# Optimization experiments

Measured on AMD Instinct MI355X. Metric: run time of the kernel, lower is better.

## Reference

```python
import jax, jax.numpy as jnp
import numpy as np

T, H, I, E, TOP_K = 4096, 2048, 768, 16, 2


def _pack_i2s(tern):
    # tern: int8 in {-1,0,1}, shape [..., K] with K % 4 == 0
    m = (tern + 1).astype(jnp.uint8)  # map to {0,1,2}
    m = m.reshape(*tern.shape[:-1], -1, 4)
    return (m[..., 0] | (m[..., 1] << 2) | (m[..., 2] << 4) | (m[..., 3] << 6)).astype(jnp.uint8)


def _quantize_alpha(alpha):
    # per-column alpha -> int8 with global scale (quantize_alpha_int8)
    scale = jnp.maximum(jnp.abs(alpha).max(), 1e-8) / 127.0
    q = jnp.clip(jnp.round(alpha / scale), -128, 127).astype(jnp.int8)
    return q, scale.astype(jnp.float32)


def _unpack_i2s(packed, K, alpha):
    # packed: uint8 [..., N, K//4]; alpha: [..., K] per input column
    shifts = jnp.array([0, 2, 4, 6], dtype=jnp.uint8)
    ext = (packed[..., None] >> shifts) & jnp.uint8(3)  # [..., N, K//4, 4]
    vals = ext.reshape(*packed.shape[:-1], K).astype(jnp.float32) - 1.0  # {-1,0,1}
    return vals * alpha[..., None, :]


def setup_inputs() -> dict:
    key = jax.random.key(0)
    ks = jax.random.split(key, 6)
    x = jax.random.normal(ks[0], (T, H), dtype=jnp.float32)
    router_logits = jax.random.normal(ks[1], (T, E), dtype=jnp.float32)
    tern13 = jax.random.randint(ks[2], (E, 2 * I, H), -1, 2, dtype=jnp.int8)
    tern2 = jax.random.randint(ks[3], (E, H, I), -1, 2, dtype=jnp.int8)
    a13 = jax.random.uniform(ks[4], (E, H), minval=0.01, maxval=0.05, dtype=jnp.float32)
    a2 = jax.random.uniform(ks[5], (E, I), minval=0.01, maxval=0.05, dtype=jnp.float32)
    w13_alpha_q, w13_alpha_scale = _quantize_alpha(a13)
    w2_alpha_q, w2_alpha_scale = _quantize_alpha(a2)
    return {
        "x": x,
        "router_logits": router_logits,
        "w13_packed": _pack_i2s(tern13),
        "w13_alpha_q": w13_alpha_q,
        "w13_alpha_scale": w13_alpha_scale,
        "w2_packed": _pack_i2s(tern2),
        "w2_alpha_q": w2_alpha_q,
        "w2_alpha_scale": w2_alpha_scale,
    }


def reference(x, router_logits, w13_packed, w13_alpha_q, w13_alpha_scale,
              w2_packed, w2_alpha_q, w2_alpha_scale):
    # dequant int8 alphas, then dequant 2-bit ternary weights
    a13 = w13_alpha_q.astype(jnp.float32) * w13_alpha_scale  # [E, H]
    a2 = w2_alpha_q.astype(jnp.float32) * w2_alpha_scale     # [E, I]
    w13 = _unpack_i2s(w13_packed, H, a13)  # [E, 2I, H]
    w2 = _unpack_i2s(w2_packed, I, a2)     # [E, H, I]

    # top-k routing with renormalized softmax weights
    probs = jax.nn.softmax(router_logits, axis=-1)
    topw, topi = jax.lax.top_k(probs, TOP_K)           # [T, k]
    topw = topw / topw.sum(axis=-1, keepdims=True)
    combine = jnp.sum(jax.nn.one_hot(topi, E, dtype=x.dtype) * topw[..., None], axis=1)  # [T, E]

    # grouped expert matmuls (dense dispatch over experts)
    gu = jnp.einsum('th,enh->ten', x, w13)             # [T, E, 2I]
    gate, up = jnp.split(gu, 2, axis=-1)
    act = jax.nn.silu(gate) * up                       # [T, E, I]
    down = jnp.einsum('tei,ehi->teh', act, w2)         # [T, E, H]
    return jnp.einsum('te,teh->th', combine, down)     # [T, H]
```

## Files before the change

kernel.cpp:

```cpp
#include <hip/hip_runtime.h>
#include <stdint.h>

#define T_TOK 4096
#define HDIM  2048
#define IDIM  768
#define NEXP  16
#define NPAIR (T_TOK * 2)
#define PAIR_CAP (NPAIR + 256)

typedef float f32x4 __attribute__((ext_vector_type(4)));
typedef __bf16 bf16x8 __attribute__((ext_vector_type(8)));
typedef unsigned short u16x8 __attribute__((ext_vector_type(8)));
typedef unsigned int u32;
typedef const __attribute__((address_space(1))) u32* as1_u32p;
typedef __attribute__((address_space(3))) u32* as3_u32p;

__device__ __forceinline__ unsigned short f2bf(float f) {
  u32 u = __float_as_uint(f);
  u += 0x7FFFu + ((u >> 16) & 1u);
  return (unsigned short)(u >> 16);
}

__device__ __forceinline__ unsigned short tb(int m) {
  return m == 0 ? (unsigned short)0xBF80 : (m == 2 ? (unsigned short)0x3F80 : (unsigned short)0);
}

__device__ __forceinline__ f32x4 mfma16(bf16x8 a, bf16x8 b, f32x4 c) {
  return __builtin_amdgcn_mfma_f32_16x16x32_bf16(a, b, c, 0, 0, 0);
}

__global__ __launch_bounds__(256) void route_kernel(
    const float* __restrict__ logits, int* __restrict__ counts,
    int* __restrict__ t2i, float* __restrict__ t2w) {
  const int t = blockIdx.x * 256 + threadIdx.x;
  if (t >= T_TOK) return;
  const float* l = logits + t * NEXP;
  float m0 = -1e30f, m1 = -1e30f;
  int i0 = 0, i1 = 0;
#pragma unroll
  for (int j = 0; j < NEXP; ++j) {
    const float v = l[j];
    if (v > m0) { m1 = m0; i1 = i0; m0 = v; i0 = j; }
    else if (v > m1) { m1 = v; i1 = j; }
  }
  const float w0 = 1.0f / (1.0f + expf(m1 - m0));
  t2i[t] = i0 | (i1 << 8);
  t2w[t] = w0;
  atomicAdd(&counts[i0], 1);
  atomicAdd(&counts[i1], 1);
}

__global__ void scan_kernel(const int* __restrict__ counts,
                            int* __restrict__ offs, int* __restrict__ cursor) {
  if (threadIdx.x == 0) {
    int s = 0;
    for (int e = 0; e < NEXP; ++e) { offs[e] = s; cursor[e] = s; s += counts[e]; }
    offs[NEXP] = s;
  }
}

__global__ __launch_bounds__(256) void fill_kernel(
    const int* __restrict__ t2i, const float* __restrict__ t2w,
    int* __restrict__ cursor, int* __restrict__ pair_token,
    float* __restrict__ pair_wt, int* __restrict__ pair_eid,
    int* __restrict__ t2p0, int* __restrict__ t2p1) {
  const int t = blockIdx.x * 256 + threadIdx.x;
  if (t >= T_TOK) return;
  const int ii = t2i[t];
  const float w0 = t2w[t];
  const int i0 = ii & 255, i1 = (ii >> 8) & 255;
  const int p0 = atomicAdd(&cursor[i0], 1);
  pair_token[p0] = t; pair_wt[p0] = w0; pair_eid[p0] = i0;
  const int p1 = atomicAdd(&cursor[i1], 1);
  pair_token[p1] = t; pair_wt[p1] = 1.0f - w0; pair_eid[p1] = i1;
  t2p0[t] = p0; t2p1[t] = p1;
}

__global__ __launch_bounds__(256) void repack_kernel(
    const int* __restrict__ w, u32* __restrict__ o) {
  const int j0 = (blockIdx.x * 256 + threadIdx.x) * 4;
  const int4* w4 = (const int4*)w;
  uint4 r;
#pragma unroll
  for (int k = 0; k < 4; ++k) {
    const int4 a = w4[j0 + k];
    ((u32*)&r)[k] = (u32)(a.x & 255) | ((u32)(a.y & 255) << 8) |
                    ((u32)(a.z & 255) << 16) | ((u32)(a.w & 255) << 24);
  }
  ((uint4*)o)[blockIdx.x * 256 + threadIdx.x] = r;
}

__global__ __launch_bounds__(256) void xg_kernel(
    const float* __restrict__ x, const int* __restrict__ a13q,
    const float* __restrict__ s13p, const int* __restrict__ pair_token,
    const int* __restrict__ pair_eid, unsigned short* __restrict__ xg) {
  const int p = blockIdx.x;
  const int t = pair_token[p];
  const int e = pair_eid[p];
  const float s13 = *s13p;
  const int h0 = threadIdx.x * 8;
  const float* xp = x + (size_t)t * HDIM + h0;
  const int* ap = a13q + (size_t)e * HDIM + h0;
  const float4 x0 = ((const float4*)xp)[0];
  const float4 x1 = ((const float4*)xp)[1];
  const int4 a0 = ((const int4*)ap)[0];
  const int4 a1 = ((const int4*)ap)[1];
  u16x8 q;
  q[0] = f2bf(x0.x * (float)a0.x * s13);
  q[1] = f2bf(x0.y * (float)a0.y * s13);
  q[2] = f2bf(x0.z * (float)a0.z * s13);
  q[3] = f2bf(x0.w * (float)a0.w * s13);
  q[4] = f2bf(x1.x * (float)a1.x * s13);
  q[5] = f2bf(x1.y * (float)a1.y * s13);
  q[6] = f2bf(x1.z * (float)a1.z * s13);
  q[7] = f2bf(x1.w * (float)a1.w * s13);
  *(u16x8*)(xg + (size_t)p * HDIM + h0) = q;
}

__global__ __launch_bounds__(256, 3) void gemm1_kernel(
    const u32* __restrict__ wq13, const int* __restrict__ a2q,
    const float* __restrict__ s2p, const int* __restrict__ counts,
    const int* __restrict__ offs, const unsigned short* __restrict__ xg,
    unsigned short* __restrict__ act) {
  const int nT = blockIdx.x;
  const int mT = blockIdx.y;
  const int e  = blockIdx.z;
  const int cnt = counts[e];
  if (mT * 128 >= cnt) return;
  const int base = offs[e];
  const int tid = threadIdx.x;

  __shared__ unsigned short sA[128 * 32];
  __shared__ unsigned short sB[128 * 40];
  __shared__ uint2 lut[256];

  {
    const int b = tid;
    const u32 lo = (u32)tb(b & 3) | ((u32)tb((b >> 2) & 3) << 16);
    const u32 hi = (u32)tb((b >> 4) & 3) | ((u32)tb((b >> 6) & 3) << 16);
    lut[b] = make_uint2(lo, hi);
  }
  __syncthreads();

  const int wave = tid >> 6, lane = tid & 63;
  const int quad = lane >> 4, ln = lane & 15;

  const int bn = tid >> 1, bhalf = tid & 1;
  const int grow = (bn < 64) ? (nT * 64 + bn) : (IDIM + nT * 64 + (bn - 64));
  const u32* bptr = wq13 + ((size_t)e * (2 * IDIM) + grow) * (HDIM / 16) + bhalf;
  unsigned short* sBw = sB + bn * 40 + (bhalf << 4);

  const int arow = lane >> 2;
  const int acol = (lane & 3) * 8;
  const size_t arow0 = (size_t)(base + mT * 128);

  f32x4 acc[2][8] = {};

  for (int kt = 0; kt < HDIM / 32; ++kt) {
#pragma unroll
    for (int c = 0; c < 2; ++c) {
      const unsigned short* gp =
          xg + (arow0 + c * 64 + wave * 16 + arow) * HDIM + kt * 32 + acol;
      unsigned short* lp = sA + (c * 64 + wave * 16) * 32;
      __builtin_amdgcn_global_load_lds((as1_u32p)(const void*)gp, (as3_u32p)(void*)lp, 16, 0, 0);
    }
    {
      const u32 wb = bptr[kt * 2];
      const uint2 q0 = lut[wb & 255], q1 = lut[(wb >> 8) & 255];
      const uint2 q2 = lut[(wb >> 16) & 255], q3 = lut[wb >> 24];
      *(uint2*)(sBw + 0) = q0;
      *(uint2*)(sBw + 4) = q1;
      *(uint2*)(sBw + 8) = q2;
      *(uint2*)(sBw + 12) = q3;
    }
    __syncthreads();
    bf16x8 af[2];
#pragma unroll
    for (int mi = 0; mi < 2; ++mi)
      af[mi] = *(const bf16x8*)(sA + (wave * 32 + mi * 16 + ln) * 32 + quad * 8);
#pragma unroll
    for (int ni = 0; ni < 8; ++ni) {
      const bf16x8 bf = *(const bf16x8*)(sB + (ni * 16 + ln) * 40 + quad * 8);
      acc[0][ni] = mfma16(af[0], bf, acc[0][ni]);
      acc[1][ni] = mfma16(af[1], bf, acc[1][ni]);
    }
    __syncthreads();
  }

  const float s2 = *s2p;
#pragma unroll
  for (int ni = 0; ni < 4; ++ni) {
    const int i = nT * 64 + ni * 16 + ln;
    const float a2v = (float)a2q[e * IDIM + i] * s2;
#pragma unroll
    for (int mi = 0; mi < 2; ++mi) {
      const f32x4 g = acc[mi][ni];
      const f32x4 u = acc[mi][ni + 4];
#pragma unroll
      for (int r = 0; r < 4; ++r) {
        const int m = mT * 128 + wave * 32 + mi * 16 + quad * 4 + r;
        if (m < cnt) {
          const float gv = g[r];
          const float av = gv / (1.0f + __expf(-gv)) * u[r];
          act[(size_t)(base + m) * IDIM + i] = f2bf(av * a2v);
        }
      }
    }
  }
}

template <bool ATOMIC>
__global__ __launch_bounds__(256, 3) void gemm2_kernel(
    const u32* __restrict__ wq2, const int* __restrict__ counts,
    const int* __restrict__ offs, const int* __restrict__ pair_token,
    const float* __restrict__ pair_wt, const unsigned short* __restrict__ act,
    float* __restrict__ dst) {
  const int nT = blockIdx.x;
  const int mT = blockIdx.y;
  const int e  = blockIdx.z;
  const int cnt = counts[e];
  if (mT * 128 >= cnt) return;
  const int base = offs[e];
  const int tid = threadIdx.x;

  __shared__ unsigned short sA[128 * 32];
  __shared__ unsigned short sB[128 * 40];
  __shared__ uint2 lut[256];
  __shared__ int stok[128];
  __shared__ float swt[128];

  {
    const int b = tid;
    const u32 lo = (u32)tb(b & 3) | ((u32)tb((b >> 2) & 3) << 16);
    const u32 hi = (u32)tb((b >> 4) & 3) | ((u32)tb((b >> 6) & 3) << 16);
    lut[b] = make_uint2(lo, hi);
    if (ATOMIC && tid < 128) {
      const int m = mT * 128 + tid;
      const bool v = m < cnt;
      stok[tid] = v ? pair_token[base + m] : 0;
      swt[tid]  = v ? pair_wt[base + m] : 0.0f;
    }
  }
  __syncthreads();

  const int wave = tid >> 6, lane = tid & 63;
  const int quad = lane >> 4, ln = lane & 15;

  const int bn = tid >> 1, bhalf = tid & 1;
  const u32* bptr = wq2 + ((size_t)e * HDIM + nT * 128 + bn) * (IDIM / 16) + bhalf;
  unsigned short* sBw = sB + bn * 40 + (bhalf << 4);

  const int arow = lane >> 2;
  const int acol = (lane & 3) * 8;
  const size_t arow0 = (size_t)(base + mT * 128);

  f32x4 acc[2][8] = {};

  for (int kt = 0; kt < IDIM / 32; ++kt) {
#pragma unroll
    for (int c = 0; c < 2; ++c) {
      const unsigned short* gp =
          act + (arow0 + c * 64 + wave * 16 + arow) * IDIM + kt * 32 + acol;
      unsigned short* lp = sA + (c * 64 + wave * 16) * 32;
      __builtin_amdgcn_global_load_lds((as1_u32p)(const void*)gp, (as3_u32p)(void*)lp, 16, 0, 0);
    }
    {
      const u32 wb = bptr[kt * 2];
      const uint2 q0 = lut[wb & 255], q1 = lut[(wb >> 8) & 255];
      const uint2 q2 = lut[(wb >> 16) & 255], q3 = lut[wb >> 24];
      *(uint2*)(sBw + 0) = q0;
      *(uint2*)(sBw + 4) = q1;
      *(uint2*)(sBw + 8) = q2;
      *(uint2*)(sBw + 12) = q3;
    }
    __syncthreads();
    bf16x8 af[2];
#pragma unroll
    for (int mi = 0; mi < 2; ++mi)
      af[mi] = *(const bf16x8*)(sA + (wave * 32 + mi * 16 + ln) * 32 + quad * 8);
#pragma unroll
    for (int ni = 0; ni < 8; ++ni) {
      const bf16x8 bf = *(const bf16x8*)(sB + (ni * 16 + ln) * 40 + quad * 8);
      acc[0][ni] = mfma16(af[0], bf, acc[0][ni]);
      acc[1][ni] = mfma16(af[1], bf, acc[1][ni]);
    }
    __syncthreads();
  }

#pragma unroll
  for (int mi = 0; mi < 2; ++mi) {
#pragma unroll
    for (int r = 0; r < 4; ++r) {
      const int ml = wave * 32 + mi * 16 + quad * 4 + r;
      const int m = mT * 128 + ml;
      if (m < cnt) {
        if (ATOMIC) {
          const float wgt = swt[ml];
          float* orow = dst + (size_t)stok[ml] * HDIM + nT * 128;
#pragma unroll
          for (int ni = 0; ni < 8; ++ni)
            atomicAdd(orow + ni * 16 + ln, wgt * acc[mi][ni][r]);
        } else {
          float* drow = dst + (size_t)(base + m) * HDIM + nT * 128;
#pragma unroll
          for (int ni = 0; ni < 8; ++ni)
            drow[ni * 16 + ln] = acc[mi][ni][r];
        }
      }
    }
  }
}

__global__ __launch_bounds__(256) void combine_kernel(
    const int* __restrict__ t2p0, const int* __restrict__ t2p1,
    const float* __restrict__ t2w, const float* __restrict__ down,
    float* __restrict__ out) {
  const int t = blockIdx.x;
  const float w0 = t2w[t];
  const float w1 = 1.0f - w0;
  const float* d0 = down + (size_t)t2p0[t] * HDIM;
  const float* d1 = down + (size_t)t2p1[t] * HDIM;
  float* o = out + (size_t)t * HDIM;
  const int h = threadIdx.x * 8;
  const f32x4 a0 = *(const f32x4*)(d0 + h);
  const f32x4 a1 = *(const f32x4*)(d0 + h + 4);
  const f32x4 b0 = *(const f32x4*)(d1 + h);
  const f32x4 b1 = *(const f32x4*)(d1 + h + 4);
  *(f32x4*)(o + h) = w0 * a0 + w1 * b0;
  *(f32x4*)(o + h + 4) = w0 * a1 + w1 * b1;
}

__global__ __launch_bounds__(256, 2) void gemm1_c(
    const int* __restrict__ w13p, const int* __restrict__ a2q,
    const float* __restrict__ s2p, const int* __restrict__ counts,
    const int* __restrict__ offs, const unsigned short* __restrict__ xg,
    unsigned short* __restrict__ act) {
  const int nT = blockIdx.x, mT = blockIdx.y, e = blockIdx.z;
  const int cnt = counts[e];
  if (mT * 256 >= cnt) return;
  const int base = offs[e];
  const int tid = threadIdx.x;
  __shared__ unsigned short sA[256 * 32];
  __shared__ unsigned short sB[128 * 40];
  __shared__ uint2 lut[256];
  {
    const int b = tid;
    const u32 lo = (u32)tb(b & 3) | ((u32)tb((b >> 2) & 3) << 16);
    const u32 hi = (u32)tb((b >> 4) & 3) | ((u32)tb((b >> 6) & 3) << 16);
    lut[b] = make_uint2(lo, hi);
  }
  __syncthreads();
  const int wave = tid >> 6, lane = tid & 63;
  const int quad = lane >> 4, ln = lane & 15;
  const int bn = tid >> 1, bhalf = tid & 1;
  const int grow = (bn < 64) ? (nT * 64 + bn) : (IDIM + nT * 64 + (bn - 64));
  const int* bptr = w13p + ((size_t)e * (2 * IDIM) + grow) * (HDIM / 4) + bhalf * 4;
  unsigned short* sBw = sB + bn * 40 + (bhalf << 4);
  const int arow = lane >> 2, acol = (lane & 3) * 8;
  const size_t arow0 = (size_t)(base + mT * 256);
  f32x4 acc[4][8] = {};
  for (int kt = 0; kt < HDIM / 32; ++kt) {
#pragma unroll
    for (int c = 0; c < 4; ++c) {
      const unsigned short* gp =
          xg + (arow0 + c * 64 + wave * 16 + arow) * HDIM + kt * 32 + acol;
      unsigned short* lp = sA + (c * 64 + wave * 16) * 32;
      __builtin_amdgcn_global_load_lds((as1_u32p)(const void*)gp, (as3_u32p)(void*)lp, 16, 0, 0);
    }
    {
      const int4 wv = *(const int4*)(bptr + kt * 8);
      const uint2 q0 = lut[wv.x], q1 = lut[wv.y], q2 = lut[wv.z], q3 = lut[wv.w];
      *(uint2*)(sBw + 0) = q0; *(uint2*)(sBw + 4) = q1;
      *(uint2*)(sBw + 8) = q2; *(uint2*)(sBw + 12) = q3;
    }
    __syncthreads();
    bf16x8 af[4];
#pragma unroll
    for (int mi = 0; mi < 4; ++mi)
      af[mi] = *(const bf16x8*)(sA + (wave * 64 + mi * 16 + ln) * 32 + quad * 8);
#pragma unroll
    for (int ni = 0; ni < 8; ++ni) {
      const bf16x8 bf = *(const bf16x8*)(sB + (ni * 16 + ln) * 40 + quad * 8);
#pragma unroll
      for (int mi = 0; mi < 4; ++mi) acc[mi][ni] = mfma16(af[mi], bf, acc[mi][ni]);
    }
    __syncthreads();
  }
  const float s2 = *s2p;
#pragma unroll
  for (int ni = 0; ni < 4; ++ni) {
    const int i = nT * 64 + ni * 16 + ln;
    const float a2v = (float)a2q[e * IDIM + i] * s2;
#pragma unroll
    for (int mi = 0; mi < 4; ++mi) {
      const f32x4 g = acc[mi][ni];
      const f32x4 u = acc[mi][ni + 4];
#pragma unroll
      for (int r = 0; r < 4; ++r) {
        const int m = mT * 256 + wave * 64 + mi * 16 + quad * 4 + r;
        if (m < cnt) {
          const float gv = g[r];
          const float av = gv / (1.0f + __expf(-gv)) * u[r];
          act[(size_t)(base + m) * IDIM + i] = f2bf(av * a2v);
        }
      }
    }
  }
}

__global__ __launch_bounds__(256, 2) void gemm2_c(
    const int* __restrict__ w2p, const int* __restrict__ counts,
    const int* __restrict__ offs, const int* __restrict__ pair_token,
    const float* __restrict__ pair_wt, const unsigned short* __restrict__ act,
    float* __restrict__ out) {
  const int nT = blockIdx.x, mT = blockIdx.y, e = blockIdx.z;
  const int cnt = counts[e];
  if (mT * 256 >= cnt) return;
  const int base = offs[e];
  const int tid = threadIdx.x;
  __shared__ unsigned short sA[256 * 32];
  __shared__ unsigned short sB[128 * 40];
  __shared__ uint2 lut[256];
  __shared__ int stok[256];
  __shared__ float swt[256];
  {
    const int b = tid;
    const u32 lo = (u32)tb(b & 3) | ((u32)tb((b >> 2) & 3) << 16);
    const u32 hi = (u32)tb((b >> 4) & 3) | ((u32)tb((b >> 6) & 3) << 16);
    lut[b] = make_uint2(lo, hi);
    const int m = mT * 256 + tid;
    const bool v = m < cnt;
    stok[tid] = v ? pair_token[base + m] : 0;
    swt[tid]  = v ? pair_wt[base + m] : 0.0f;
  }
  __syncthreads();
  const int wave = tid >> 6, lane = tid & 63;
  const int quad = lane >> 4, ln = lane & 15;
  const int bn = tid >> 1, bhalf = tid & 1;
  const int* bptr = w2p + ((size_t)e * HDIM + nT * 128 + bn) * (IDIM / 4) + bhalf * 4;
  unsigned short* sBw = sB + bn * 40 + (bhalf << 4);
  const int arow = lane >> 2, acol = (lane & 3) * 8;
  const size_t arow0 = (size_t)(base + mT * 256);
  f32x4 acc[4][8] = {};
  for (int kt = 0; kt < IDIM / 32; ++kt) {
#pragma unroll
    for (int c = 0; c < 4; ++c) {
      const unsigned short* gp =
          act + (arow0 + c * 64 + wave * 16 + arow) * IDIM + kt * 32 + acol;
      unsigned short* lp = sA + (c * 64 + wave * 16) * 32;
      __builtin_amdgcn_global_load_lds((as1_u32p)(const void*)gp, (as3_u32p)(void*)lp, 16, 0, 0);
    }
    {
      const int4 wv = *(const int4*)(bptr + kt * 8);
      const uint2 q0 = lut[wv.x], q1 = lut[wv.y], q2 = lut[wv.z], q3 = lut[wv.w];
      *(uint2*)(sBw + 0) = q0; *(uint2*)(sBw + 4) = q1;
      *(uint2*)(sBw + 8) = q2; *(uint2*)(sBw + 12) = q3;
    }
    __syncthreads();
    bf16x8 af[4];
#pragma unroll
    for (int mi = 0; mi < 4; ++mi)
      af[mi] = *(const bf16x8*)(sA + (wave * 64 + mi * 16 + ln) * 32 + quad * 8);
#pragma unroll
    for (int ni = 0; ni < 8; ++ni) {
      const bf16x8 bf = *(const bf16x8*)(sB + (ni * 16 + ln) * 40 + quad * 8);
#pragma unroll
      for (int mi = 0; mi < 4; ++mi) acc[mi][ni] = mfma16(af[mi], bf, acc[mi][ni]);
    }
    __syncthreads();
  }
#pragma unroll
  for (int mi = 0; mi < 4; ++mi) {
#pragma unroll
    for (int r = 0; r < 4; ++r) {
      const int ml = wave * 64 + mi * 16 + quad * 4 + r;
      const int m = mT * 256 + ml;
      if (m < cnt) {
        const float wgt = swt[ml];
        float* orow = out + (size_t)stok[ml] * HDIM + nT * 128;
#pragma unroll
        for (int ni = 0; ni < 8; ++ni)
          atomicAdd(orow + ni * 16 + ln, wgt * acc[mi][ni][r]);
      }
    }
  }
}

extern "C" void kernel_launch(void* const* d_in, const int* in_sizes, int n_in,
                              void* d_out, int out_size, void* d_ws, size_t ws_size,
                              hipStream_t stream) {
  const float* x      = (const float*)d_in[0];
  const float* logits = (const float*)d_in[1];
  const int*   w13p   = (const int*)d_in[2];
  const int*   a13q   = (const int*)d_in[3];
  const float* s13    = (const float*)d_in[4];
  const int*   w2p    = (const int*)d_in[5];
  const int*   a2q    = (const int*)d_in[6];
  const float* s2     = (const float*)d_in[7];
  float* out = (float*)d_out;

  char* ws = (char*)d_ws;
  int*   counts     = (int*)(ws + 0);
  int*   cursor     = (int*)(ws + 64);
  int*   offs       = (int*)(ws + 128);
  int*   t2i        = (int*)(ws + 256);
  float* t2w        = (float*)(ws + 256 + 4 * T_TOK);
  int*   t2p0       = (int*)(ws + 256 + 8 * T_TOK);
  int*   t2p1       = (int*)(ws + 256 + 12 * T_TOK);
  int*   pair_token = (int*)(ws + 256 + 16 * T_TOK);
  float* pair_wt    = (float*)(ws + 256 + 16 * T_TOK + 4 * PAIR_CAP);
  int*   pair_eid   = (int*)(ws + 256 + 16 * T_TOK + 8 * PAIR_CAP);
  const size_t hdr_end = ((size_t)(256 + 16 * T_TOK + 12 * PAIR_CAP) + 255) & ~(size_t)255;

  const size_t n32_13 = (size_t)NEXP * 2 * IDIM * (HDIM / 16);
  const size_t n32_2  = (size_t)NEXP * HDIM * (IDIM / 16);
  const size_t rp13_b = n32_13 * 4, rp2_b = n32_2 * 4;
  const size_t xg_b   = (size_t)PAIR_CAP * HDIM * 2;
  const size_t act_b  = (size_t)PAIR_CAP * IDIM * 2;
  const size_t down_b = (size_t)PAIR_CAP * HDIM * 4;

  const size_t need_A = hdr_end + rp13_b + rp2_b + xg_b + act_b + down_b;
  const size_t need_B = hdr_end + rp13_b + rp2_b + xg_b + act_b;

  hipMemsetAsync(counts, 0, 256, stream);
  route_kernel<<<T_TOK / 256, 256, 0, stream>>>(logits, counts, t2i, t2w);
  scan_kernel<<<1, 64, 0, stream>>>(counts, offs, cursor);
  fill_kernel<<<T_TOK / 256, 256, 0, stream>>>(t2i, t2w, cursor, pair_token, pair_wt,
                                               pair_eid, t2p0, t2p1);

  if (ws_size >= need_B) {
    u32* rp13 = (u32*)(ws + hdr_end);
    u32* rp2  = (u32*)(ws + hdr_end + rp13_b);
    unsigned short* xg  = (unsigned short*)(ws + hdr_end + rp13_b + rp2_b);
    unsigned short* act = (unsigned short*)(ws + hdr_end + rp13_b + rp2_b + xg_b);
    repack_kernel<<<(int)(n32_13 / 1024), 256, 0, stream>>>(w13p, rp13);
    repack_kernel<<<(int)(n32_2 / 1024), 256, 0, stream>>>(w2p, rp2);
    xg_kernel<<<NPAIR, 256, 0, stream>>>(x, a13q, s13, pair_token, pair_eid, xg);
    gemm1_kernel<<<dim3(12, 32, 16), 256, 0, stream>>>(rp13, a2q, s2, counts, offs, xg, act);
    if (ws_size >= need_A) {
      float* down = (float*)(ws + need_B);
      gemm2_kernel<false><<<dim3(16, 32, 16), 256, 0, stream>>>(
          rp2, counts, offs, pair_token, pair_wt, act, down);
      combine_kernel<<<T_TOK, 256, 0, stream>>>(t2p0, t2p1, t2w, down, out);
    } else {
      hipMemsetAsync(out, 0, (size_t)out_size * sizeof(float), stream);
      gemm2_kernel<true><<<dim3(16, 32, 16), 256, 0, stream>>>(
          rp2, counts, offs, pair_token, pair_wt, act, out);
    }
  } else {
    unsigned short* xg  = (unsigned short*)(ws + hdr_end);
    unsigned short* act = (unsigned short*)(ws + hdr_end + xg_b);
    hipMemsetAsync(out, 0, (size_t)out_size * sizeof(float), stream);
    xg_kernel<<<NPAIR, 256, 0, stream>>>(x, a13q, s13, pair_token, pair_eid, xg);
    gemm1_c<<<dim3(12, 16, 16), 256, 0, stream>>>(w13p, a2q, s2, counts, offs, xg, act);
    gemm2_c<<<dim3(16, 16, 16), 256, 0, stream>>>(w2p, counts, offs, pair_token,
                                                  pair_wt, act, out);
  }
}
```

Baseline: 390.6 us.

## Use 2x2 wave tiling, XCD-aware block order, bf16 down buffer, fold routing weight

The GEMM kernels now split the 128x128 tile across waves in a 2x2 grid, so each wave does 4x4 MFMAs per k-step instead of 2x8 with more A/B fragment reuse. Blocks are launched on a flat grid remapped so tiles of the same expert spread across XCDs. Weight words are loaded as uint4 every other k-step, and the LDS B row stride changes from 40 to 36. The routing weight moves into gemm1's activation epilogue, and the down buffer is stored as bf16 so combine becomes a plain add. The fallback path without repacking is removed. Storing down in bf16 adds a rounding step, and occupancy hints rise from 3 to 4 blocks.

```diff
diff --git a/kernel.cpp b/kernel.cpp
--- a/kernel.cpp
+++ b/kernel.cpp
@@ -117,21 +117,23 @@
   *(u16x8*)(xg + (size_t)p * HDIM + h0) = q;
 }
 
-__global__ __launch_bounds__(256, 3) void gemm1_kernel(
+__global__ __launch_bounds__(256, 4) void gemm1_kernel(
     const u32* __restrict__ wq13, const int* __restrict__ a2q,
     const float* __restrict__ s2p, const int* __restrict__ counts,
-    const int* __restrict__ offs, const unsigned short* __restrict__ xg,
-    unsigned short* __restrict__ act) {
-  const int nT = blockIdx.x;
-  const int mT = blockIdx.y;
-  const int e  = blockIdx.z;
+    const int* __restrict__ offs, const float* __restrict__ pair_wt,
+    const unsigned short* __restrict__ xg, unsigned short* __restrict__ act) {
+  const int id = blockIdx.x;
+  const int xcd = id & 7, sblk = id >> 3;
+  const int nT = sblk % 12;
+  const int gg = (sblk / 12) * 8 + xcd;
+  const int e = gg & 15, mT = gg >> 4;
   const int cnt = counts[e];
   if (mT * 128 >= cnt) return;
   const int base = offs[e];
   const int tid = threadIdx.x;
 
   __shared__ unsigned short sA[128 * 32];
-  __shared__ unsigned short sB[128 * 40];
+  __shared__ unsigned short sB[128 * 36 + 8];
   __shared__ uint2 lut[256];
 
   {
@@ -143,29 +145,32 @@
   __syncthreads();
 
   const int wave = tid >> 6, lane = tid & 63;
+  const int wm = wave >> 1, wn = wave & 1;
   const int quad = lane >> 4, ln = lane & 15;
 
   const int bn = tid >> 1, bhalf = tid & 1;
   const int grow = (bn < 64) ? (nT * 64 + bn) : (IDIM + nT * 64 + (bn - 64));
-  const u32* bptr = wq13 + ((size_t)e * (2 * IDIM) + grow) * (HDIM / 16) + bhalf;
-  unsigned short* sBw = sB + bn * 40 + (bhalf << 4);
+  const u32* browp = wq13 + ((size_t)e * (2 * IDIM) + grow) * (HDIM / 16);
+  unsigned short* sBw = sB + bn * 36 + (bhalf << 4);
 
   const int arow = lane >> 2;
   const int acol = (lane & 3) * 8;
   const size_t arow0 = (size_t)(base + mT * 128);
 
-  f32x4 acc[2][8] = {};
+  f32x4 acc[4][4] = {};
+  uint4 bq;
 
   for (int kt = 0; kt < HDIM / 32; ++kt) {
+    if ((kt & 1) == 0) bq = *(const uint4*)(browp + kt * 2);
 #pragma unroll
     for (int c = 0; c < 2; ++c) {
       const unsigned short* gp =
-          xg + (arow0 + c * 64 + wave * 16 + arow) * HDIM + kt * 32 + acol;
-      unsigned short* lp = sA + (c * 64 + wave * 16) * 32;
+          xg + (arow0 + wave * 32 + c * 16 + arow) * HDIM + kt * 32 + acol;
+      unsigned short* lp = sA + (wave * 32 + c * 16) * 32;
       __builtin_amdgcn_global_load_lds((as1_u32p)(const void*)gp, (as3_u32p)(void*)lp, 16, 0, 0);
     }
     {
-      const u32 wb = bptr[kt * 2];
+      const u32 wb = (kt & 1) ? (bhalf ? bq.w : bq.z) : (bhalf ? bq.y : bq.x);
       const uint2 q0 = lut[wb & 255], q1 = lut[(wb >> 8) & 255];
       const uint2 q2 = lut[(wb >> 16) & 255], q3 = lut[wb >> 24];
       *(uint2*)(sBw + 0) = q0;
@@ -174,35 +179,39 @@
       *(uint2*)(sBw + 12) = q3;
     }
     __syncthreads();
-    bf16x8 af[2];
-#pragma unroll
-    for (int mi = 0; mi < 2; ++mi)
-      af[mi] = *(const bf16x8*)(sA + (wave * 32 + mi * 16 + ln) * 32 + quad * 8);
-#pragma unroll
-    for (int ni = 0; ni < 8; ++ni) {
-      const bf16x8 bf = *(const bf16x8*)(sB + (ni * 16 + ln) * 40 + quad * 8);
-      acc[0][ni] = mfma16(af[0], bf, acc[0][ni]);
-      acc[1][ni] = mfma16(af[1], bf, acc[1][ni]);
-    }
+    bf16x8 af[4], bf[4];
+#pragma unroll
+    for (int mi = 0; mi < 4; ++mi)
+      af[mi] = *(const bf16x8*)(sA + (wm * 64 + mi * 16 + ln) * 32 + quad * 8);
+#pragma unroll
+    for (int ni = 0; ni < 4; ++ni) {
+      const int brow = (ni < 2) ? (wn * 32 + ni * 16) : (64 + wn * 32 + (ni - 2) * 16);
+      bf[ni] = *(const bf16x8*)(sB + (brow + ln) * 36 + quad * 8);
+    }
+#pragma unroll
+    for (int ni = 0; ni < 4; ++ni)
+#pragma unroll
+      for (int mi = 0; mi < 4; ++mi) acc[mi][ni] = mfma16(af[mi], bf[ni], acc[mi][ni]);
     __syncthreads();
   }
 
   const float s2 = *s2p;
 #pragma unroll
-  for (int ni = 0; ni < 4; ++ni) {
-    const int i = nT * 64 + ni * 16 + ln;
+  for (int gi = 0; gi < 2; ++gi) {
+    const int i = nT * 64 + wn * 32 + gi * 16 + ln;
     const float a2v = (float)a2q[e * IDIM + i] * s2;
 #pragma unroll
-    for (int mi = 0; mi < 2; ++mi) {
-      const f32x4 g = acc[mi][ni];
-      const f32x4 u = acc[mi][ni + 4];
+    for (int mi = 0; mi < 4; ++mi) {
+      const f32x4 g = acc[mi][gi];
+      const f32x4 u = acc[mi][gi + 2];
 #pragma unroll
       for (int r = 0; r < 4; ++r) {
-        const int m = mT * 128 + wave * 32 + mi * 16 + quad * 4 + r;
+        const int m = mT * 128 + wm * 64 + mi * 16 + quad * 4 + r;
         if (m < cnt) {
+          const float wt = pair_wt[base + m];
           const float gv = g[r];
-          const float av = gv / (1.0f + __expf(-gv)) * u[r];
-          act[(size_t)(base + m) * IDIM + i] = f2bf(av * a2v);
+          const float av = gv / (1.0f + __expf(-gv)) * u[r] * a2v * wt;
+          act[(size_t)(base + m) * IDIM + i] = f2bf(av);
         }
       }
     }
@@ -210,24 +219,25 @@
 }
 
 template <bool ATOMIC>
-__global__ __launch_bounds__(256, 3) void gemm2_kernel(
+__global__ __launch_bounds__(256, 4) void gemm2_kernel(
     const u32* __restrict__ wq2, const int* __restrict__ counts,
     const int* __restrict__ offs, const int* __restrict__ pair_token,
-    const float* __restrict__ pair_wt, const unsigned short* __restrict__ act,
-    float* __restrict__ dst) {
-  const int nT = blockIdx.x;
-  const int mT = blockIdx.y;
-  const int e  = blockIdx.z;
+    const unsigned short* __restrict__ act, float* __restrict__ outp,
+    unsigned short* __restrict__ down) {
+  const int id = blockIdx.x;
+  const int xcd = id & 7, sblk = id >> 3;
+  const int nT = sblk & 15;
+  const int gg = (sblk >> 4) * 8 + xcd;
+  const int e = gg & 15, mT = gg >> 4;
   const int cnt = counts[e];
   if (mT * 128 >= cnt) return;
   const int base = offs[e];
   const int tid = threadIdx.x;
 
   __shared__ unsigned short sA[128 * 32];
-  __shared__ unsigned short sB[128 * 40];
+  __shared__ unsigned short sB[128 * 36 + 8];
   __shared__ uint2 lut[256];
   __shared__ int stok[128];
-  __shared__ float swt[128];
 
   {
     const int b = tid;
@@ -236,36 +246,37 @@
     lut[b] = make_uint2(lo, hi);
     if (ATOMIC && tid < 128) {
       const int m = mT * 128 + tid;
-      const bool v = m < cnt;
-      stok[tid] = v ? pair_token[base + m] : 0;
-      swt[tid]  = v ? pair_wt[base + m] : 0.0f;
+      stok[tid] = (m < cnt) ? pair_token[base + m] : 0;
     }
   }
   __syncthreads();
 
   const int wave = tid >> 6, lane = tid & 63;
+  const int wm = wave >> 1, wn = wave & 1;
   const int quad = lane >> 4, ln = lane & 15;
 
   const int bn = tid >> 1, bhalf = tid & 1;
-  const u32* bptr = wq2 + ((size_t)e * HDIM + nT * 128 + bn) * (IDIM / 16) + bhalf;
-  unsigned short* sBw = sB + bn * 40 + (bhalf << 4);
+  const u32* browp = wq2 + ((size_t)e * HDIM + nT * 128 + bn) * (IDIM / 16);
+  unsigned short* sBw = sB + bn * 36 + (bhalf << 4);
 
   const int arow = lane >> 2;
   const int acol = (lane & 3) * 8;
   const size_t arow0 = (size_t)(base + mT * 128);
 
-  f32x4 acc[2][8] = {};
+  f32x4 acc[4][4] = {};
+  uint4 bq;
 
   for (int kt = 0; kt < IDIM / 32; ++kt) {
+    if ((kt & 1) == 0) bq = *(const uint4*)(browp + kt * 2);
 #pragma unroll
     for (int c = 0; c < 2; ++c) {
       const unsigned short* gp =
-          act + (arow0 + c * 64 + wave * 16 + arow) * IDIM + kt * 32 + acol;
-      unsigned short* lp = sA + (c * 64 + wave * 16) * 32;
+          act + (arow0 + wave * 32 + c * 16 + arow) * IDIM + kt * 32 + acol;
+      unsigned short* lp = sA + (wave * 32 + c * 16) * 32;
       __builtin_amdgcn_global_load_lds((as1_u32p)(const void*)gp, (as3_u32p)(void*)lp, 16, 0, 0);
     }
     {
-      const u32 wb = bptr[kt * 2];
+      const u32 wb = (kt & 1) ? (bhalf ? bq.w : bq.z) : (bhalf ? bq.y : bq.x);
       const uint2 q0 = lut[wb & 255], q1 = lut[(wb >> 8) & 255];
       const uint2 q2 = lut[(wb >> 16) & 255], q3 = lut[wb >> 24];
       *(uint2*)(sBw + 0) = q0;
@@ -274,37 +285,38 @@
       *(uint2*)(sBw + 12) = q3;
     }
     __syncthreads();
-    bf16x8 af[2];
-#pragma unroll
-    for (int mi = 0; mi < 2; ++mi)
-      af[mi] = *(const bf16x8*)(sA + (wave * 32 + mi * 16 + ln) * 32 + quad * 8);
-#pragma unroll
-    for (int ni = 0; ni < 8; ++ni) {
-      const bf16x8 bf = *(const bf16x8*)(sB + (ni * 16 + ln) * 40 + quad * 8);
-      acc[0][ni] = mfma16(af[0], bf, acc[0][ni]);
-      acc[1][ni] = mfma16(af[1], bf, acc[1][ni]);
-    }
+    bf16x8 af[4], bf[4];
+#pragma unroll
+    for (int mi = 0; mi < 4; ++mi)
+      af[mi] = *(const bf16x8*)(sA + (wm * 64 + mi * 16 + ln) * 32 + quad * 8);
+#pragma unroll
+    for (int ni = 0; ni < 4; ++ni)
+      bf[ni] = *(const bf16x8*)(sB + (wn * 64 + ni * 16 + ln) * 36 + quad * 8);
+#pragma unroll
+    for (int ni = 0; ni < 4; ++ni)
+#pragma unroll
+      for (int mi = 0; mi < 4; ++mi) acc[mi][ni] = mfma16(af[mi], bf[ni], acc[mi][ni]);
     __syncthreads();
   }
 
 #pragma unroll
-  for (int mi = 0; mi < 2; ++mi) {
+  for (int mi = 0; mi < 4; ++mi) {
 #pragma unroll
     for (int r = 0; r < 4; ++r) {
-      const int ml = wave * 32 + mi * 16 + quad * 4 + r;
+      const int ml = wm * 64 + mi * 16 + quad * 4 + r;
       const int m = mT * 128 + ml;
       if (m < cnt) {
+        const int col0 = nT * 128 + wn * 64;
         if (ATOMIC) {
-          const float wgt = swt[ml];
-          float* orow = dst + (size_t)stok[ml] * HDIM + nT * 128;
-#pragma unroll
-          for (int ni = 0; ni < 8; ++ni)
-            atomicAdd(orow + ni * 16 + ln, wgt * acc[mi][ni][r]);
+          float* orow = outp + (size_t)stok[ml] * HDIM + col0;
+#pragma unroll
+          for (int ni = 0; ni < 4; ++ni)
+            atomicAdd(orow + ni * 16 + ln, acc[mi][ni][r]);
         } else {
-          float* drow = dst + (size_t)(base + m) * HDIM + nT * 128;
-#pragma unroll
-          for (int ni = 0; ni < 8; ++ni)
-            drow[ni * 16 + ln] = acc[mi][ni][r];
+          unsigned short* drow = down + (size_t)(base + m) * HDIM + col0;
+#pragma unroll
+          for (int ni = 0; ni < 4; ++ni)
+            drow[ni * 16 + ln] = f2bf(acc[mi][ni][r]);
         }
       }
     }
@@ -313,177 +325,20 @@
 
 __global__ __launch_bounds__(256) void combine_kernel(
     const int* __restrict__ t2p0, const int* __restrict__ t2p1,
-    const float* __restrict__ t2w, const float* __restrict__ down,
-    float* __restrict__ out) {
+    const unsigned short* __restrict__ down, float* __restrict__ out) {
   const int t = blockIdx.x;
-  const float w0 = t2w[t];
-  const float w1 = 1.0f - w0;
-  const float* d0 = down + (size_t)t2p0[t] * HDIM;
-  const float* d1 = down + (size_t)t2p1[t] * HDIM;
-  float* o = out + (size_t)t * HDIM;
   const int h = threadIdx.x * 8;
-  const f32x4 a0 = *(const f32x4*)(d0 + h);
-  const f32x4 a1 = *(const f32x4*)(d0 + h + 4);
-  const f32x4 b0 = *(const f32x4*)(d1 + h);
-  const f32x4 b1 = *(const f32x4*)(d1 + h + 4);
-  *(f32x4*)(o + h) = w0 * a0 + w1 * b0;
-  *(f32x4*)(o + h + 4) = w0 * a1 + w1 * b1;
-}
-
-__global__ __launch_bounds__(256, 2) void gemm1_c(
-    const int* __restrict__ w13p, const int* __restrict__ a2q,
-    const float* __restrict__ s2p, const int* __restrict__ counts,
-    const int* __restrict__ offs, const unsigned short* __restrict__ xg,
-    unsigned short* __restrict__ act) {
-  const int nT = blockIdx.x, mT = blockIdx.y, e = blockIdx.z;
-  const int cnt = counts[e];
-  if (mT * 256 >= cnt) return;
-  const int base = offs[e];
-  const int tid = threadIdx.x;
-  __shared__ unsigned short sA[256 * 32];
-  __shared__ unsigned short sB[128 * 40];
-  __shared__ uint2 lut[256];
-  {
-    const int b = tid;
-    const u32 lo = (u32)tb(b & 3) | ((u32)tb((b >> 2) & 3) << 16);
-    const u32 hi = (u32)tb((b >> 4) & 3) | ((u32)tb((b >> 6) & 3) << 16);
-    lut[b] = make_uint2(lo, hi);
-  }
-  __syncthreads();
-  const int wave = tid >> 6, lane = tid & 63;
-  const int quad = lane >> 4, ln = lane & 15;
-  const int bn = tid >> 1, bhalf = tid & 1;
-  const int grow = (bn < 64) ? (nT * 64 + bn) : (IDIM + nT * 64 + (bn - 64));
-  const int* bptr = w13p + ((size_t)e * (2 * IDIM) + grow) * (HDIM / 4) + bhalf * 4;
-  unsigned short* sBw = sB + bn * 40 + (bhalf << 4);
-  const int arow = lane >> 2, acol = (lane & 3) * 8;
-  const size_t arow0 = (size_t)(base + mT * 256);
-  f32x4 acc[4][8] = {};
-  for (int kt = 0; kt < HDIM / 32; ++kt) {
-#pragma unroll
-    for (int c = 0; c < 4; ++c) {
-      const unsigned short* gp =
-          xg + (arow0 + c * 64 + wave * 16 + arow) * HDIM + kt * 32 + acol;
-      unsigned short* lp = sA + (c * 64 + wave * 16) * 32;
-      __builtin_amdgcn_global_load_lds((as1_u32p)(const void*)gp, (as3_u32p)(void*)lp, 16, 0, 0);
-    }
-    {
-      const int4 wv = *(const int4*)(bptr + kt * 8);
-      const uint2 q0 = lut[wv.x], q1 = lut[wv.y], q2 = lut[wv.z], q3 = lut[wv.w];
-      *(uint2*)(sBw + 0) = q0; *(uint2*)(sBw + 4) = q1;
-      *(uint2*)(sBw + 8) = q2; *(uint2*)(sBw + 12) = q3;
-    }
-    __syncthreads();
-    bf16x8 af[4];
-#pragma unroll
-    for (int mi = 0; mi < 4; ++mi)
-      af[mi] = *(const bf16x8*)(sA + (wave * 64 + mi * 16 + ln) * 32 + quad * 8);
-#pragma unroll
-    for (int ni = 0; ni < 8; ++ni) {
-      const bf16x8 bf = *(const bf16x8*)(sB + (ni * 16 + ln) * 40 + quad * 8);
-#pragma unroll
-      for (int mi = 0; mi < 4; ++mi) acc[mi][ni] = mfma16(af[mi], bf, acc[mi][ni]);
-    }
-    __syncthreads();
-  }
-  const float s2 = *s2p;
-#pragma unroll
-  for (int ni = 0; ni < 4; ++ni) {
-    const int i = nT * 64 + ni * 16 + ln;
-    const float a2v = (float)a2q[e * IDIM + i] * s2;
-#pragma unroll
-    for (int mi = 0; mi < 4; ++mi) {
-      const f32x4 g = acc[mi][ni];
-      const f32x4 u = acc[mi][ni + 4];
-#pragma unroll
-      for (int r = 0; r < 4; ++r) {
-        const int m = mT * 256 + wave * 64 + mi * 16 + quad * 4 + r;
-        if (m < cnt) {
-          const float gv = g[r];
-          const float av = gv / (1.0f + __expf(-gv)) * u[r];
-          act[(size_t)(base + m) * IDIM + i] = f2bf(av * a2v);
-        }
-      }
-    }
-  }
-}
-
-__global__ __launch_bounds__(256, 2) void gemm2_c(
-    const int* __restrict__ w2p, const int* __restrict__ counts,
-    const int* __restrict__ offs, const int* __restrict__ pair_token,
-    const float* __restrict__ pair_wt, const unsigned short* __restrict__ act,
-    float* __restrict__ out) {
-  const int nT = blockIdx.x, mT = blockIdx.y, e = blockIdx.z;
-  const int cnt = counts[e];
-  if (mT * 256 >= cnt) return;
-  const int base = offs[e];
-  const int tid = threadIdx.x;
-  __shared__ unsigned short sA[256 * 32];
-  __shared__ unsigned short sB[128 * 40];
-  __shared__ uint2 lut[256];
-  __shared__ int stok[256];
-  __shared__ float swt[256];
-  {
-    const int b = tid;
-    const u32 lo = (u32)tb(b & 3) | ((u32)tb((b >> 2) & 3) << 16);
-    const u32 hi = (u32)tb((b >> 4) & 3) | ((u32)tb((b >> 6) & 3) << 16);
-    lut[b] = make_uint2(lo, hi);
-    const int m = mT * 256 + tid;
-    const bool v = m < cnt;
-    stok[tid] = v ? pair_token[base + m] : 0;
-    swt[tid]  = v ? pair_wt[base + m] : 0.0f;
-  }
-  __syncthreads();
-  const int wave = tid >> 6, lane = tid & 63;
-  const int quad = lane >> 4, ln = lane & 15;
-  const int bn = tid >> 1, bhalf = tid & 1;
-  const int* bptr = w2p + ((size_t)e * HDIM + nT * 128 + bn) * (IDIM / 4) + bhalf * 4;
-  unsigned short* sBw = sB + bn * 40 + (bhalf << 4);
-  const int arow = lane >> 2, acol = (lane & 3) * 8;
-  const size_t arow0 = (size_t)(base + mT * 256);
-  f32x4 acc[4][8] = {};
-  for (int kt = 0; kt < IDIM / 32; ++kt) {
-#pragma unroll
-    for (int c = 0; c < 4; ++c) {
-      const unsigned short* gp =
-          act + (arow0 + c * 64 + wave * 16 + arow) * IDIM + kt * 32 + acol;
-      unsigned short* lp = sA + (c * 64 + wave * 16) * 32;
-      __builtin_amdgcn_global_load_lds((as1_u32p)(const void*)gp, (as3_u32p)(void*)lp, 16, 0, 0);
-    }
-    {
-      const int4 wv = *(const int4*)(bptr + kt * 8);
-      const uint2 q0 = lut[wv.x], q1 = lut[wv.y], q2 = lut[wv.z], q3 = lut[wv.w];
-      *(uint2*)(sBw + 0) = q0; *(uint2*)(sBw + 4) = q1;
-      *(uint2*)(sBw + 8) = q2; *(uint2*)(sBw + 12) = q3;
-    }
-    __syncthreads();
-    bf16x8 af[4];
-#pragma unroll
-    for (int mi = 0; mi < 4; ++mi)
-      af[mi] = *(const bf16x8*)(sA + (wave * 64 + mi * 16 + ln) * 32 + quad * 8);
-#pragma unroll
-    for (int ni = 0; ni < 8; ++ni) {
-      const bf16x8 bf = *(const bf16x8*)(sB + (ni * 16 + ln) * 40 + quad * 8);
-#pragma unroll
-      for (int mi = 0; mi < 4; ++mi) acc[mi][ni] = mfma16(af[mi], bf, acc[mi][ni]);
-    }
-    __syncthreads();
-  }
-#pragma unroll
-  for (int mi = 0; mi < 4; ++mi) {
-#pragma unroll
-    for (int r = 0; r < 4; ++r) {
-      const int ml = wave * 64 + mi * 16 + quad * 4 + r;
-      const int m = mT * 256 + ml;
-      if (m < cnt) {
-        const float wgt = swt[ml];
-        float* orow = out + (size_t)stok[ml] * HDIM + nT * 128;
-#pragma unroll
-        for (int ni = 0; ni < 8; ++ni)
-          atomicAdd(orow + ni * 16 + ln, wgt * acc[mi][ni][r]);
-      }
-    }
-  }
+  const u16x8 a = *(const u16x8*)(down + (size_t)t2p0[t] * HDIM + h);
+  const u16x8 b = *(const u16x8*)(down + (size_t)t2p1[t] * HDIM + h);
+  f32x4 o0, o1;
+#pragma unroll
+  for (int j = 0; j < 4; ++j) {
+    o0[j] = __uint_as_float((u32)a[j] << 16) + __uint_as_float((u32)b[j] << 16);
+    o1[j] = __uint_as_float((u32)a[j + 4] << 16) + __uint_as_float((u32)b[j + 4] << 16);
+  }
+  float* o = out + (size_t)t * HDIM + h;
+  *(f32x4*)(o) = o0;
+  *(f32x4*)(o + 4) = o1;
 }
 
 extern "C" void kernel_launch(void* const* d_in, const int* in_sizes, int n_in,
@@ -517,43 +372,35 @@
   const size_t rp13_b = n32_13 * 4, rp2_b = n32_2 * 4;
   const size_t xg_b   = (size_t)PAIR_CAP * HDIM * 2;
   const size_t act_b  = (size_t)PAIR_CAP * IDIM * 2;
-  const size_t down_b = (size_t)PAIR_CAP * HDIM * 4;
-
-  const size_t need_A = hdr_end + rp13_b + rp2_b + xg_b + act_b + down_b;
+  const size_t dwn_b  = (size_t)PAIR_CAP * HDIM * 2;
+
   const size_t need_B = hdr_end + rp13_b + rp2_b + xg_b + act_b;
+  const size_t need_A = need_B + dwn_b;
+
+  u32* rp13 = (u32*)(ws + hdr_end);
+  u32* rp2  = (u32*)(ws + hdr_end + rp13_b);
+  unsigned short* xg  = (unsigned short*)(ws + hdr_end + rp13_b + rp2_b);
+  unsigned short* act = (unsigned short*)(ws + hdr_end + rp13_b + rp2_b + xg_b);
 
   hipMemsetAsync(counts, 0, 256, stream);
   route_kernel<<<T_TOK / 256, 256, 0, stream>>>(logits, counts, t2i, t2w);
   scan_kernel<<<1, 64, 0, stream>>>(counts, offs, cursor);
   fill_kernel<<<T_TOK / 256, 256, 0, stream>>>(t2i, t2w, cursor, pair_token, pair_wt,
                                                pair_eid, t2p0, t2p1);
-
-  if (ws_size >= need_B) {
-    u32* rp13 = (u32*)(ws + hdr_end);
-    u32* rp2  = (u32*)(ws + hdr_end + rp13_b);
-    unsigned short* xg  = (unsigned short*)(ws + hdr_end + rp13_b + rp2_b);
-    unsigned short* act = (unsigned short*)(ws + hdr_end + rp13_b + rp2_b + xg_b);
-    repack_kernel<<<(int)(n32_13 / 1024), 256, 0, stream>>>(w13p, rp13);
-    repack_kernel<<<(int)(n32_2 / 1024), 256, 0, stream>>>(w2p, rp2);
-    xg_kernel<<<NPAIR, 256, 0, stream>>>(x, a13q, s13, pair_token, pair_eid, xg);
-    gemm1_kernel<<<dim3(12, 32, 16), 256, 0, stream>>>(rp13, a2q, s2, counts, offs, xg, act);
-    if (ws_size >= need_A) {
-      float* down = (float*)(ws + need_B);
-      gemm2_kernel<false><<<dim3(16, 32, 16), 256, 0, stream>>>(
-          rp2, counts, offs, pair_token, pair_wt, act, down);
-      combine_kernel<<<T_TOK, 256, 0, stream>>>(t2p0, t2p1, t2w, down, out);
-    } else {
-      hipMemsetAsync(out, 0, (size_t)out_size * sizeof(float), stream);
-      gemm2_kernel<true><<<dim3(16, 32, 16), 256, 0, stream>>>(
-          rp2, counts, offs, pair_token, pair_wt, act, out);
-    }
+  repack_kernel<<<(int)(n32_13 / 1024), 256, 0, stream>>>(w13p, rp13);
+  repack_kernel<<<(int)(n32_2 / 1024), 256, 0, stream>>>(w2p, rp2);
+  xg_kernel<<<NPAIR, 256, 0, stream>>>(x, a13q, s13, pair_token, pair_eid, xg);
+
+  gemm1_kernel<<<6144, 256, 0, stream>>>(rp13, a2q, s2, counts, offs, pair_wt, xg, act);
+
+  if (ws_size >= need_A) {
+    unsigned short* down = (unsigned short*)(ws + need_B);
+    gemm2_kernel<false><<<8192, 256, 0, stream>>>(rp2, counts, offs, pair_token,
+                                                  act, nullptr, down);
+    combine_kernel<<<T_TOK, 256, 0, stream>>>(t2p0, t2p1, down, out);
   } else {
-    unsigned short* xg  = (unsigned short*)(ws + hdr_end);
-    unsigned short* act = (unsigned short*)(ws + hdr_end + xg_b);
     hipMemsetAsync(out, 0, (size_t)out_size * sizeof(float), stream);
-    xg_kernel<<<NPAIR, 256, 0, stream>>>(x, a13q, s13, pair_token, pair_eid, xg);
-    gemm1_c<<<dim3(12, 16, 16), 256, 0, stream>>>(w13p, a2q, s2, counts, offs, xg, act);
-    gemm2_c<<<dim3(16, 16, 16), 256, 0, stream>>>(w2p, counts, offs, pair_token,
-                                                  pair_wt, act, out);
-  }
-}
+    gemm2_kernel<true><<<8192, 256, 0, stream>>>(rp2, counts, offs, pair_token,
+                                                 act, out, nullptr);
+  }
+}
```

Measured after the change: 351.1 us. 1.11x faster.
